# Kernel tuning notes

Measured on AMD Instinct MI355X. Metric: run time of the kernel, lower is better.

## Reference

```python
import jax, jax.numpy as jnp
import numpy as np

DIM = 1024
E = 8
K = 2
EPS = 1e-5

def _ln(x, g, b):
    mu = jnp.mean(x, axis=-1, keepdims=True)
    var = jnp.mean(jnp.square(x - mu), axis=-1, keepdims=True)
    return (x - mu) * jax.lax.rsqrt(var + EPS) * g + b

def setup_inputs() -> dict:
    key = jax.random.key(0)
    ks = jax.random.split(key, 8)
    H = 2 * DIM
    s_in = 1.0 / np.sqrt(DIM)
    s_h = 1.0 / np.sqrt(H)
    return {
        "x": jax.random.normal(ks[0], (2, 2048, DIM), dtype=jnp.float32),
        "gate_w": jax.random.uniform(ks[1], (DIM, E), minval=-s_in, maxval=s_in, dtype=jnp.float32),
        "w1": jax.random.uniform(ks[2], (E, DIM, H), minval=-s_in, maxval=s_in, dtype=jnp.float32),
        "b1": jax.random.uniform(ks[3], (E, H), minval=-s_in, maxval=s_in, dtype=jnp.float32),
        "ln1_g": jnp.ones((E, H), dtype=jnp.float32),
        "ln1_b": jnp.zeros((E, H), dtype=jnp.float32),
        "w2": jax.random.uniform(ks[4], (E, H, DIM), minval=-s_h, maxval=s_h, dtype=jnp.float32),
        "b2": jax.random.uniform(ks[5], (E, DIM), minval=-s_h, maxval=s_h, dtype=jnp.float32),
        "ln_g": jnp.ones((DIM,), dtype=jnp.float32),
        "ln_b": jnp.zeros((DIM,), dtype=jnp.float32),
    }

def reference(x, gate_w, w1, b1, ln1_g, ln1_b, w2, b2, ln_g, ln_b):
    shape = x.shape
    xf = x.reshape(-1, shape[-1])                      # [T, D]
    gates = jax.nn.softmax(xf @ gate_w, axis=-1)       # [T, E]
    topw, topi = jax.lax.top_k(gates, K)               # [T, K]
    topw = topw / jnp.sum(topw, axis=-1, keepdims=True)
    # combine weights per expert: [T, E]
    combine = jnp.sum(topw[:, :, None] * jax.nn.one_hot(topi, E, dtype=xf.dtype), axis=1)
    # run all experts on all tokens (vectorized grouped GEMM), combine by gate mask
    h = jnp.einsum('td,edh->teh', xf, w1) + b1          # [T, E, 2D]
    h = _ln(h, ln1_g, ln1_b)
    h = jax.nn.gelu(h, approximate=False)
    y = jnp.einsum('teh,ehd->ted', h, w2) + b2          # [T, E, D]
    out = jnp.einsum('ted,te->td', y, combine)          # [T, D]
    out = _ln(out + xf, ln_g, ln_b)
    return out.reshape(shape)
```

## Files before the change

### kernel.cpp

```cpp
#include <hip/hip_runtime.h>
#include <hip/hip_bf16.h>

#define DIMX 1024
#define HID  2048
#define NE   8
#define NT   4096
#define NPAIR 8192
#define MAXSTRIP 72

typedef __attribute__((ext_vector_type(8))) __bf16 bf16x8;
typedef __attribute__((ext_vector_type(4))) float f32x4;

__device__ inline unsigned short f2bf(float f) {
  union { float f; unsigned u; } v; v.f = f;
  unsigned r = v.u + 0x7FFFu + ((v.u >> 16) & 1u);
  return (unsigned short)(r >> 16);
}
__device__ inline float bf2f(unsigned short h) {
  union { unsigned u; float f; } v; v.u = ((unsigned)h) << 16;
  return v.f;
}

__device__ __forceinline__ void gload_lds16(const unsigned short* g, unsigned short* l) {
  __builtin_amdgcn_global_load_lds(
      (const __attribute__((address_space(1))) unsigned int*)g,
      (__attribute__((address_space(3))) unsigned int*)l, 16, 0, 0);
}

#define O_CNT   0u
#define O_TOK   1024u
#define O_TK    132096u
#define O_PW    263168u
#define O_TI    394240u
#define O_TW    427008u
#define O_POFF  459776u
#define O_SE    459904u
#define O_SR0   460416u
#define O_XBF   524288u
#define O_W1T   16777216u
#define O_W2T   50331648u
#define O_H     83886080u
#define O_Y     121634816u

__global__ __launch_bounds__(256) void k_gate_cvt(const float* __restrict__ x,
                                                  const float* __restrict__ gw,
                                                  unsigned short* __restrict__ xbf,
                                                  int* __restrict__ ti,
                                                  float* __restrict__ tw) {
  int t = blockIdx.x * 4 + (threadIdx.x >> 6);
  int lane = threadIdx.x & 63;
  const float4* xr = (const float4*)(x + (size_t)t * DIMX);
  ushort4* xo = (ushort4*)(xbf + (size_t)t * DIMX);
  float p[NE];
#pragma unroll
  for (int e = 0; e < NE; e++) p[e] = 0.f;
#pragma unroll
  for (int j = 0; j < 4; j++) {
    int idx4 = j * 64 + lane;
    float4 v = xr[idx4];
    ushort4 o; o.x = f2bf(v.x); o.y = f2bf(v.y); o.z = f2bf(v.z); o.w = f2bf(v.w);
    xo[idx4] = o;
    const float4* gp = (const float4*)(gw + (size_t)(idx4 * 4) * NE);
    float4 gA = gp[0], gB = gp[1], gC = gp[2], gD = gp[3];
    float4 gE = gp[4], gF = gp[5], gG = gp[6], gH = gp[7];
    p[0] += v.x * gA.x + v.y * gC.x + v.z * gE.x + v.w * gG.x;
    p[1] += v.x * gA.y + v.y * gC.y + v.z * gE.y + v.w * gG.y;
    p[2] += v.x * gA.z + v.y * gC.z + v.z * gE.z + v.w * gG.z;
    p[3] += v.x * gA.w + v.y * gC.w + v.z * gE.w + v.w * gG.w;
    p[4] += v.x * gB.x + v.y * gD.x + v.z * gF.x + v.w * gH.x;
    p[5] += v.x * gB.y + v.y * gD.y + v.z * gF.y + v.w * gH.y;
    p[6] += v.x * gB.z + v.y * gD.z + v.z * gF.z + v.w * gH.z;
    p[7] += v.x * gB.w + v.y * gD.w + v.z * gF.w + v.w * gH.w;
  }
#pragma unroll
  for (int e = 0; e < NE; e++)
#pragma unroll
    for (int off = 32; off > 0; off >>= 1) p[e] += __shfl_xor(p[e], off);
  if (lane == 0) {
    int ia = 0; float va = p[0];
#pragma unroll
    for (int e = 1; e < NE; e++) if (p[e] > va) { va = p[e]; ia = e; }
    int ib = -1; float vb = -3.0e38f;
#pragma unroll
    for (int e = 0; e < NE; e++) { if (e == ia) continue; if (p[e] > vb) { vb = p[e]; ib = e; } }
    float w0 = 1.f / (1.f + expf(vb - va));
    ti[t * 2] = ia;     tw[t * 2] = w0;
    ti[t * 2 + 1] = ib; tw[t * 2 + 1] = 1.f - w0;
  }
}

__global__ __launch_bounds__(512) void k_build(const int* __restrict__ ti,
                                               const float* __restrict__ tw,
                                               int* __restrict__ cnt,
                                               int* __restrict__ poffs,
                                               int* __restrict__ s_e, int* __restrict__ s_r0,
                                               int* __restrict__ ptok, int* __restrict__ ptk,
                                               float* __restrict__ pw) {
  __shared__ int sti[NPAIR];
  __shared__ float stw[NPAIR];
  __shared__ int scnt[NE];
  for (int i = threadIdx.x; i < NPAIR; i += 512) { sti[i] = ti[i]; stw[i] = tw[i]; }
  __syncthreads();
  int wid = threadIdx.x >> 6;
  int lane = threadIdx.x & 63;
  int c = 0;
  for (int p = lane; p < NPAIR; p += 64) c += (sti[p] == wid) ? 1 : 0;
#pragma unroll
  for (int off = 32; off > 0; off >>= 1) c += __shfl_xor(c, off);
  if (lane == 0) scnt[wid] = c;
  __syncthreads();
  if (threadIdx.x == 0) {
    int s = 0, pacc = 0;
    for (int e = 0; e < NE; e++) {
      cnt[e] = scnt[e];
      poffs[e] = pacc;
      int ns = (scnt[e] + 127) >> 7;
      for (int k = 0; k < ns; k++) { s_e[s] = e; s_r0[s] = k * 128; s++; }
      pacc += ns * 128;
    }
    poffs[NE] = pacc;
    for (; s < MAXSTRIP; s++) { s_e[s] = -1; s_r0[s] = 0; }
  }
  int base = 0;
  for (int p0 = 0; p0 < NPAIR; p0 += 64) {
    int p = p0 + lane;
    bool m = (sti[p] == wid);
    unsigned long long mask = __ballot(m);
    if (m) {
      int pos = base + __popcll(mask & ((1ull << lane) - 1ull));
      ptok[wid * NT + pos] = p >> 1;
      ptk[wid * NT + pos] = p;
      pw[wid * NT + pos] = stw[p];
    }
    base += __popcll(mask);
  }
}

__global__ __launch_bounds__(256) void k_transpose_cvt(const float* __restrict__ in,
                                                       unsigned short* __restrict__ out,
                                                       int R, int C) {
  __shared__ float tile[64][73];
  int e = blockIdx.z;
  const float* ip = in + (size_t)e * R * C;
  unsigned short* op = out + (size_t)e * R * C;
  int c0 = blockIdx.x * 64, r0 = blockIdx.y * 64;
  int tx = threadIdx.x & 15, ty = threadIdx.x >> 4;
#pragma unroll
  for (int i = 0; i < 4; i++) {
    int row = ty + i * 16;
    float4 v = *(const float4*)(ip + (size_t)(r0 + row) * C + c0 + tx * 4);
    tile[row][tx * 4] = v.x; tile[row][tx * 4 + 1] = v.y;
    tile[row][tx * 4 + 2] = v.z; tile[row][tx * 4 + 3] = v.w;
  }
  __syncthreads();
  int rx = threadIdx.x & 15, cy = threadIdx.x >> 4;
  int r_off = rx * 4;
#pragma unroll
  for (int i = 0; i < 4; i++) {
    int cc = cy + i * 16;
    ushort4 h;
    h.x = f2bf(tile[r_off][cc]);     h.y = f2bf(tile[r_off + 1][cc]);
    h.z = f2bf(tile[r_off + 2][cc]); h.w = f2bf(tile[r_off + 3][cc]);
    *(ushort4*)(op + (size_t)(c0 + cc) * R + r0 + r_off) = h;
  }
}

#define BM 128
#define BN 128
#define BK 32
#define KSTEPS 32

__global__ __launch_bounds__(256) void k_gemm1(
    const unsigned short* __restrict__ xbf,
    const unsigned short* __restrict__ w1t,
    const float* __restrict__ bias1,
    const int* __restrict__ cnt, const int* __restrict__ s_e,
    const int* __restrict__ s_r0, const int* __restrict__ poffs,
    const int* __restrict__ ptok,
    unsigned short* __restrict__ hpre)
{
  int lid = blockIdx.x + 16 * blockIdx.y;
  int xcd = lid & 7;
  int t4 = lid >> 3;
  int colb = t4 & 15;
  int s = xcd * 9 + (t4 >> 4);
  int e = s_e[s];
  if (e < 0) return;
  int r0e = s_r0[s];
  int n_e = cnt[e];
  int pbase = poffs[e];
  int col0 = colb * BN;

  __shared__ __align__(16) unsigned short As[3][BM][BK];
  __shared__ __align__(16) unsigned short Bs[3][BN][BK];

  int tid = threadIdx.x;
  int lane = tid & 63, wid = tid >> 6;
  int wr = wid >> 1, wc = wid & 1;
  int quad = lane >> 4, m16 = lane & 15;

  int rr = lane >> 2;
  int csrc = ((lane & 3) ^ ((lane >> 3) & 3)) * 8;
  int ga0 = r0e + wid * 32 + rr;      if (ga0 >= n_e) ga0 = n_e - 1;
  int ga1 = r0e + wid * 32 + 16 + rr; if (ga1 >= n_e) ga1 = n_e - 1;
  int t0 = ptok[e * NT + ga0];
  int t1 = ptok[e * NT + ga1];
  const unsigned short* a0p = xbf + (size_t)t0 * DIMX + csrc;
  const unsigned short* a1p = xbf + (size_t)t1 * DIMX + csrc;
  const unsigned short* bbase = w1t + (size_t)e * HID * DIMX;
  const unsigned short* b0p = bbase + (size_t)(col0 + wid * 32 + rr) * DIMX + csrc;
  const unsigned short* b1p = bbase + (size_t)(col0 + wid * 32 + 16 + rr) * DIMX + csrc;

  int ca = (quad ^ ((m16 >> 1) & 3)) * 8;

  f32x4 acc[4][4];
#pragma unroll
  for (int i = 0; i < 4; i++)
#pragma unroll
    for (int j = 0; j < 4; j++) acc[i][j] = (f32x4)(0.f);

#define STAGE1(b, kk) do { \
    gload_lds16(a0p + (kk), &As[b][wid * 32][0]); \
    gload_lds16(a1p + (kk), &As[b][wid * 32 + 16][0]); \
    gload_lds16(b0p + (kk), &Bs[b][wid * 32][0]); \
    gload_lds16(b1p + (kk), &Bs[b][wid * 32 + 16][0]); \
  } while (0)

  STAGE1(0, 0);
  int cur = 0;
  for (int k = 0; k < KSTEPS; ++k) {
    int nxt = (cur == 2) ? 0 : cur + 1;
    if (k + 1 < KSTEPS) {
      STAGE1(nxt, (k + 1) * BK);
      asm volatile("s_waitcnt vmcnt(4)" ::: "memory");
    } else {
      asm volatile("s_waitcnt vmcnt(0)" ::: "memory");
    }
    asm volatile("s_waitcnt lgkmcnt(0)" ::: "memory");
    __builtin_amdgcn_sched_barrier(0);
    __builtin_amdgcn_s_barrier();
    __builtin_amdgcn_sched_barrier(0);
    bf16x8 af[4], bfr[4];
#pragma unroll
    for (int i = 0; i < 4; i++) af[i]  = *(const bf16x8*)&As[cur][wr * 64 + i * 16 + m16][ca];
#pragma unroll
    for (int j = 0; j < 4; j++) bfr[j] = *(const bf16x8*)&Bs[cur][wc * 64 + j * 16 + m16][ca];
    __builtin_amdgcn_s_setprio(1);
#pragma unroll
    for (int i = 0; i < 4; i++)
#pragma unroll
      for (int j = 0; j < 4; j++)
        acc[i][j] = __builtin_amdgcn_mfma_f32_16x16x32_bf16(af[i], bfr[j], acc[i][j], 0, 0, 0);
    __builtin_amdgcn_s_setprio(0);
    cur = nxt;
  }
#undef STAGE1

  float bj[4];
#pragma unroll
  for (int j = 0; j < 4; j++) bj[j] = bias1[e * HID + col0 + wc * 64 + j * 16 + m16];
#pragma unroll
  for (int i = 0; i < 4; i++) {
#pragma unroll
    for (int r = 0; r < 4; r++) {
      int g = r0e + wr * 64 + i * 16 + quad * 4 + r;
      if (g < n_e) {
        size_t rowbase = (size_t)(pbase + g) * HID;
#pragma unroll
        for (int j = 0; j < 4; j++) {
          int colg = col0 + wc * 64 + j * 16 + m16;
          hpre[rowbase + colg] = f2bf(acc[i][j][r] + bj[j]);
        }
      }
    }
  }
}

__global__ __launch_bounds__(256) void k_ln_gelu(unsigned short* __restrict__ h,
                                                 const float* __restrict__ g1,
                                                 const float* __restrict__ bb1,
                                                 const int* __restrict__ s_e) {
  int row = blockIdx.x * 4 + (threadIdx.x >> 6);
  int e = s_e[row >> 7];
  if (e < 0) return;
  int lane = threadIdx.x & 63;
  unsigned short* p = h + (size_t)row * HID;
  int4* p4 = (int4*)p;
  int4 raw[4];
#pragma unroll
  for (int sg = 0; sg < 4; sg++) raw[sg] = p4[sg * 64 + lane];
  float v[32];
#pragma unroll
  for (int sg = 0; sg < 4; sg++) {
    const unsigned short* u = (const unsigned short*)&raw[sg];
#pragma unroll
    for (int k = 0; k < 8; k++) v[sg * 8 + k] = bf2f(u[k]);
  }
  float s = 0.f;
#pragma unroll
  for (int i = 0; i < 32; i++) s += v[i];
#pragma unroll
  for (int off = 32; off > 0; off >>= 1) s += __shfl_xor(s, off);
  float mean = s * (1.f / HID);
  float sq = 0.f;
#pragma unroll
  for (int i = 0; i < 32; i++) { float d = v[i] - mean; sq += d * d; }
#pragma unroll
  for (int off = 32; off > 0; off >>= 1) sq += __shfl_xor(sq, off);
  float rstd = rsqrtf(sq * (1.f / HID) + 1e-5f);
  const float4* gg = (const float4*)(g1 + (size_t)e * HID);
  const float4* gb = (const float4*)(bb1 + (size_t)e * HID);
#pragma unroll
  for (int sg = 0; sg < 4; sg++) {
    float4 ga = gg[sg * 128 + lane * 2], gc = gg[sg * 128 + lane * 2 + 1];
    float4 ba = gb[sg * 128 + lane * 2], bc = gb[sg * 128 + lane * 2 + 1];
    float gn[8] = {ga.x, ga.y, ga.z, ga.w, gc.x, gc.y, gc.z, gc.w};
    float bn[8] = {ba.x, ba.y, ba.z, ba.w, bc.x, bc.y, bc.z, bc.w};
    unsigned short o[8];
#pragma unroll
    for (int k = 0; k < 8; k++) {
      float xn = (v[sg * 8 + k] - mean) * rstd * gn[k] + bn[k];
      float ge = 0.5f * xn * (1.f + erff(xn * 0.7071067811865476f));
      o[k] = f2bf(ge);
    }
    p4[sg * 64 + lane] = *(const int4*)o;
  }
}

__global__ __launch_bounds__(256) void k_gemm2(
    const unsigned short* __restrict__ hb,
    const unsigned short* __restrict__ w2t,
    const float* __restrict__ bias2,
    const int* __restrict__ cnt, const int* __restrict__ s_e,
    const int* __restrict__ s_r0, const int* __restrict__ poffs,
    const int* __restrict__ ptk, const float* __restrict__ pw,
    float* __restrict__ ybufA, float* __restrict__ ybufB)
{
  int lid = blockIdx.x + 8 * (blockIdx.y + 72 * blockIdx.z);
  int xcd = lid & 7;
  int t4 = lid >> 3;
  int colb = t4 & 7;
  int rem = t4 >> 3;
  int ks = rem & 1;
  int s = xcd * 9 + (rem >> 1);
  int e = s_e[s];
  if (e < 0) return;
  int r0e = s_r0[s];
  int n_e = cnt[e];
  int pbase = poffs[e];
  int col0 = colb * BN;
  int kbase = ks << 10;

  __shared__ __align__(16) unsigned short As[3][BM][BK];
  __shared__ __align__(16) unsigned short Bs[3][BN][BK];

  int tid = threadIdx.x;
  int lane = tid & 63, wid = tid >> 6;
  int wr = wid >> 1, wc = wid & 1;
  int quad = lane >> 4, m16 = lane & 15;

  int rr = lane >> 2;
  int csrc = ((lane & 3) ^ ((lane >> 3) & 3)) * 8;
  int ga0 = r0e + wid * 32 + rr;      if (ga0 >= n_e) ga0 = n_e - 1;
  int ga1 = r0e + wid * 32 + 16 + rr; if (ga1 >= n_e) ga1 = n_e - 1;
  const unsigned short* a0p = hb + (size_t)(pbase + ga0) * HID + kbase + csrc;
  const unsigned short* a1p = hb + (size_t)(pbase + ga1) * HID + kbase + csrc;
  const unsigned short* bbase = w2t + (size_t)e * DIMX * HID;
  const unsigned short* b0p = bbase + (size_t)(col0 + wid * 32 + rr) * HID + kbase + csrc;
  const unsigned short* b1p = bbase + (size_t)(col0 + wid * 32 + 16 + rr) * HID + kbase + csrc;

  int ca = (quad ^ ((m16 >> 1) & 3)) * 8;

  f32x4 acc[4][4];
#pragma unroll
  for (int i = 0; i < 4; i++)
#pragma unroll
    for (int j = 0; j < 4; j++) acc[i][j] = (f32x4)(0.f);

#define STAGE2(b, kk) do { \
    gload_lds16(a0p + (kk), &As[b][wid * 32][0]); \
    gload_lds16(a1p + (kk), &As[b][wid * 32 + 16][0]); \
    gload_lds16(b0p + (kk), &Bs[b][wid * 32][0]); \
    gload_lds16(b1p + (kk), &Bs[b][wid * 32 + 16][0]); \
  } while (0)

  STAGE2(0, 0);
  int cur = 0;
  for (int k = 0; k < KSTEPS; ++k) {
    int nxt = (cur == 2) ? 0 : cur + 1;
    if (k + 1 < KSTEPS) {
      STAGE2(nxt, (k + 1) * BK);
      asm volatile("s_waitcnt vmcnt(4)" ::: "memory");
    } else {
      asm volatile("s_waitcnt vmcnt(0)" ::: "memory");
    }
    asm volatile("s_waitcnt lgkmcnt(0)" ::: "memory");
    __builtin_amdgcn_sched_barrier(0);
    __builtin_amdgcn_s_barrier();
    __builtin_amdgcn_sched_barrier(0);
    bf16x8 af[4], bfr[4];
#pragma unroll
    for (int i = 0; i < 4; i++) af[i]  = *(const bf16x8*)&As[cur][wr * 64 + i * 16 + m16][ca];
#pragma unroll
    for (int j = 0; j < 4; j++) bfr[j] = *(const bf16x8*)&Bs[cur][wc * 64 + j * 16 + m16][ca];
    __builtin_amdgcn_s_setprio(1);
#pragma unroll
    for (int i = 0; i < 4; i++)
#pragma unroll
      for (int j = 0; j < 4; j++)
        acc[i][j] = __builtin_amdgcn_mfma_f32_16x16x32_bf16(af[i], bfr[j], acc[i][j], 0, 0, 0);
    __builtin_amdgcn_s_setprio(0);
    cur = nxt;
  }
#undef STAGE2

  float* yb = ks ? ybufB : ybufA;
  float bj[4];
#pragma unroll
  for (int j = 0; j < 4; j++)
    bj[j] = ks ? bias2[e * DIMX + col0 + wc * 64 + j * 16 + m16] : 0.f;
#pragma unroll
  for (int i = 0; i < 4; i++) {
#pragma unroll
    for (int r = 0; r < 4; r++) {
      int g = r0e + wr * 64 + i * 16 + quad * 4 + r;
      if (g < n_e) {
        int pi = e * NT + g;
        float w = pw[pi];
        size_t obase = (size_t)ptk[pi] * DIMX;
#pragma unroll
        for (int j = 0; j < 4; j++) {
          int colg = col0 + wc * 64 + j * 16 + m16;
          yb[obase + colg] = (acc[i][j][r] + bj[j]) * w;
        }
      }
    }
  }
}

__global__ __launch_bounds__(256) void k_final(const float* __restrict__ ybA,
                                               const float* __restrict__ ybB,
                                               const float* __restrict__ x,
                                               const float* __restrict__ lg,
                                               const float* __restrict__ lb,
                                               float* __restrict__ out) {
  int t = blockIdx.x * 4 + (threadIdx.x >> 6);
  int lane = threadIdx.x & 63;
  const float4* yA0 = (const float4*)(ybA + (size_t)t * 2 * DIMX);
  const float4* yA1 = yA0 + DIMX / 4;
  const float4* yB0 = (const float4*)(ybB + (size_t)t * 2 * DIMX);
  const float4* yB1 = yB0 + DIMX / 4;
  const float4* x4 = (const float4*)(x + (size_t)t * DIMX);
  float4 v[4];
  float s = 0.f;
#pragma unroll
  for (int sg = 0; sg < 4; sg++) {
    int idx = sg * 64 + lane;
    float4 a = yA0[idx], b = yA1[idx], a2 = yB0[idx], b2 = yB1[idx], c = x4[idx];
    v[sg].x = a.x + b.x + a2.x + b2.x + c.x;
    v[sg].y = a.y + b.y + a2.y + b2.y + c.y;
    v[sg].z = a.z + b.z + a2.z + b2.z + c.z;
    v[sg].w = a.w + b.w + a2.w + b2.w + c.w;
    s += v[sg].x + v[sg].y + v[sg].z + v[sg].w;
  }
#pragma unroll
  for (int off = 32; off > 0; off >>= 1) s += __shfl_xor(s, off);
  float mean = s * (1.f / DIMX);
  float sq = 0.f;
#pragma unroll
  for (int sg = 0; sg < 4; sg++) {
    float dx = v[sg].x - mean, dy = v[sg].y - mean, dz = v[sg].z - mean, dw = v[sg].w - mean;
    sq += dx * dx + dy * dy + dz * dz + dw * dw;
  }
#pragma unroll
  for (int off = 32; off > 0; off >>= 1) sq += __shfl_xor(sq, off);
  float rstd = rsqrtf(sq * (1.f / DIMX) + 1e-5f);
  float4* o4 = (float4*)(out + (size_t)t * DIMX);
#pragma unroll
  for (int sg = 0; sg < 4; sg++) {
    int idx = sg * 64 + lane;
    float4 g = ((const float4*)lg)[idx], bb = ((const float4*)lb)[idx];
    float4 o;
    o.x = (v[sg].x - mean) * rstd * g.x + bb.x;
    o.y = (v[sg].y - mean) * rstd * g.y + bb.y;
    o.z = (v[sg].z - mean) * rstd * g.z + bb.z;
    o.w = (v[sg].w - mean) * rstd * g.w + bb.w;
    o4[idx] = o;
  }
}

extern "C" void kernel_launch(void* const* d_in, const int* in_sizes, int n_in,
                              void* d_out, int out_size, void* d_ws, size_t ws_size,
                              hipStream_t stream) {
  const float* x     = (const float*)d_in[0];
  const float* gw    = (const float*)d_in[1];
  const float* w1    = (const float*)d_in[2];
  const float* b1    = (const float*)d_in[3];
  const float* ln1g  = (const float*)d_in[4];
  const float* ln1b  = (const float*)d_in[5];
  const float* w2    = (const float*)d_in[6];
  const float* b2    = (const float*)d_in[7];
  const float* lng   = (const float*)d_in[8];
  const float* lnb   = (const float*)d_in[9];
  float* out = (float*)d_out;

  char* ws = (char*)d_ws;
  int* cnt   = (int*)(ws + O_CNT);
  int* ptok  = (int*)(ws + O_TOK);
  int* ptk   = (int*)(ws + O_TK);
  float* pw  = (float*)(ws + O_PW);
  int* ti    = (int*)(ws + O_TI);
  float* tw  = (float*)(ws + O_TW);
  int* poffs = (int*)(ws + O_POFF);
  int* s_e   = (int*)(ws + O_SE);
  int* s_r0  = (int*)(ws + O_SR0);
  unsigned short* xbf  = (unsigned short*)(ws + O_XBF);
  unsigned short* w1t  = (unsigned short*)(ws + O_W1T);
  unsigned short* w2t  = (unsigned short*)(ws + O_W2T);
  unsigned short* hpre = (unsigned short*)(ws + O_H);
  float* ybufA = (float*)(ws + O_Y);
  float* ybufB = (float*)(ws + O_W1T);

  hipLaunchKernelGGL(k_gate_cvt, dim3(NT / 4), dim3(256), 0, stream, x, gw, xbf, ti, tw);
  hipLaunchKernelGGL(k_build, dim3(1), dim3(512), 0, stream, ti, tw, cnt, poffs, s_e, s_r0,
                     ptok, ptk, pw);
  hipLaunchKernelGGL(k_transpose_cvt, dim3(HID / 64, DIMX / 64, NE), dim3(256), 0, stream,
                     w1, w1t, DIMX, HID);
  hipLaunchKernelGGL(k_transpose_cvt, dim3(DIMX / 64, HID / 64, NE), dim3(256), 0, stream,
                     w2, w2t, HID, DIMX);
  hipLaunchKernelGGL(k_gemm1, dim3(HID / BN, MAXSTRIP), dim3(256), 0, stream,
                     xbf, w1t, b1, cnt, s_e, s_r0, poffs, ptok, hpre);
  hipLaunchKernelGGL(k_ln_gelu, dim3(MAXSTRIP * BM / 4), dim3(256), 0, stream,
                     hpre, ln1g, ln1b, s_e);
  hipLaunchKernelGGL(k_gemm2, dim3(DIMX / BN, MAXSTRIP, 2), dim3(256), 0, stream,
                     hpre, w2t, b2, cnt, s_e, s_r0, poffs, ptk, pw, ybufA, ybufB);
  hipLaunchKernelGGL(k_final, dim3(NT / 4), dim3(256), 0, stream, ybufA, ybufB, x, lng, lnb, out);
}
```

Measured before the change: 375.3 us.

## Double K tile to 64 with double-buffered LDS pipeline in both GEMMs

Both grouped GEMM kernels now use a K tile of 64 with two LDS buffers instead of 32 with three. The global-to-LDS load pattern and the XOR swizzle are reworked for 8-row groups, and each iteration issues two MFMA half-steps. This halves the number of barrier/waitcnt iterations and raises MFMA work per sync. In exchange there is less prefetch depth, an extra barrier before each stage, and the LDS footprint grows from 48KB to 64KB, which may reduce occupancy.

```diff
diff --git a/kernel.cpp b/kernel.cpp
--- a/kernel.cpp
+++ b/kernel.cpp
@@ -167,8 +167,8 @@
 
 #define BM 128
 #define BN 128
-#define BK 32
-#define KSTEPS 32
+#define BK 64
+#define KSTEPS 16
 
 __global__ __launch_bounds__(256) void k_gemm1(
     const unsigned short* __restrict__ xbf,
@@ -191,27 +191,29 @@
   int pbase = poffs[e];
   int col0 = colb * BN;
 
-  __shared__ __align__(16) unsigned short As[3][BM][BK];
-  __shared__ __align__(16) unsigned short Bs[3][BN][BK];
+  __shared__ __align__(16) unsigned short As[2][BM][BK];
+  __shared__ __align__(16) unsigned short Bs[2][BN][BK];
 
   int tid = threadIdx.x;
   int lane = tid & 63, wid = tid >> 6;
   int wr = wid >> 1, wc = wid & 1;
   int quad = lane >> 4, m16 = lane & 15;
 
-  int rr = lane >> 2;
-  int csrc = ((lane & 3) ^ ((lane >> 3) & 3)) * 8;
-  int ga0 = r0e + wid * 32 + rr;      if (ga0 >= n_e) ga0 = n_e - 1;
-  int ga1 = r0e + wid * 32 + 16 + rr; if (ga1 >= n_e) ga1 = n_e - 1;
-  int t0 = ptok[e * NT + ga0];
-  int t1 = ptok[e * NT + ga1];
-  const unsigned short* a0p = xbf + (size_t)t0 * DIMX + csrc;
-  const unsigned short* a1p = xbf + (size_t)t1 * DIMX + csrc;
-  const unsigned short* bbase = w1t + (size_t)e * HID * DIMX;
-  const unsigned short* b0p = bbase + (size_t)(col0 + wid * 32 + rr) * DIMX + csrc;
-  const unsigned short* b1p = bbase + (size_t)(col0 + wid * 32 + 16 + rr) * DIMX + csrc;
-
-  int ca = (quad ^ ((m16 >> 1) & 3)) * 8;
+  int r8 = lane >> 3;
+  int csrc = ((lane & 7) ^ r8) * 8;
+  const unsigned short* ap[4];
+  const unsigned short* bp[4];
+  {
+    const unsigned short* bbase = w1t + (size_t)e * HID * DIMX;
+#pragma unroll
+    for (int i = 0; i < 4; i++) {
+      int ga = r0e + wid * 32 + i * 8 + r8; if (ga >= n_e) ga = n_e - 1;
+      ap[i] = xbf + (size_t)ptok[e * NT + ga] * DIMX + csrc;
+      bp[i] = bbase + (size_t)(col0 + wid * 32 + i * 8 + r8) * DIMX + csrc;
+    }
+  }
+
+  int ca0 = (quad ^ (m16 & 7)) * 8;
 
   f32x4 acc[4][4];
 #pragma unroll
@@ -220,31 +222,36 @@
     for (int j = 0; j < 4; j++) acc[i][j] = (f32x4)(0.f);
 
 #define STAGE1(b, kk) do { \
-    gload_lds16(a0p + (kk), &As[b][wid * 32][0]); \
-    gload_lds16(a1p + (kk), &As[b][wid * 32 + 16][0]); \
-    gload_lds16(b0p + (kk), &Bs[b][wid * 32][0]); \
-    gload_lds16(b1p + (kk), &Bs[b][wid * 32 + 16][0]); \
+    gload_lds16(ap[0] + (kk), &As[b][wid * 32 +  0][0]); \
+    gload_lds16(ap[1] + (kk), &As[b][wid * 32 +  8][0]); \
+    gload_lds16(ap[2] + (kk), &As[b][wid * 32 + 16][0]); \
+    gload_lds16(ap[3] + (kk), &As[b][wid * 32 + 24][0]); \
+    gload_lds16(bp[0] + (kk), &Bs[b][wid * 32 +  0][0]); \
+    gload_lds16(bp[1] + (kk), &Bs[b][wid * 32 +  8][0]); \
+    gload_lds16(bp[2] + (kk), &Bs[b][wid * 32 + 16][0]); \
+    gload_lds16(bp[3] + (kk), &Bs[b][wid * 32 + 24][0]); \
   } while (0)
 
   STAGE1(0, 0);
   int cur = 0;
   for (int k = 0; k < KSTEPS; ++k) {
-    int nxt = (cur == 2) ? 0 : cur + 1;
+    asm volatile("s_waitcnt lgkmcnt(0)" ::: "memory");
+    __builtin_amdgcn_sched_barrier(0);
+    __builtin_amdgcn_s_barrier();
     if (k + 1 < KSTEPS) {
-      STAGE1(nxt, (k + 1) * BK);
-      asm volatile("s_waitcnt vmcnt(4)" ::: "memory");
+      STAGE1(cur ^ 1, (k + 1) * BK);
+      asm volatile("s_waitcnt vmcnt(8)" ::: "memory");
     } else {
       asm volatile("s_waitcnt vmcnt(0)" ::: "memory");
     }
-    asm volatile("s_waitcnt lgkmcnt(0)" ::: "memory");
     __builtin_amdgcn_sched_barrier(0);
     __builtin_amdgcn_s_barrier();
     __builtin_amdgcn_sched_barrier(0);
     bf16x8 af[4], bfr[4];
 #pragma unroll
-    for (int i = 0; i < 4; i++) af[i]  = *(const bf16x8*)&As[cur][wr * 64 + i * 16 + m16][ca];
-#pragma unroll
-    for (int j = 0; j < 4; j++) bfr[j] = *(const bf16x8*)&Bs[cur][wc * 64 + j * 16 + m16][ca];
+    for (int i = 0; i < 4; i++) af[i]  = *(const bf16x8*)&As[cur][wr * 64 + i * 16 + m16][ca0];
+#pragma unroll
+    for (int j = 0; j < 4; j++) bfr[j] = *(const bf16x8*)&Bs[cur][wc * 64 + j * 16 + m16][ca0];
     __builtin_amdgcn_s_setprio(1);
 #pragma unroll
     for (int i = 0; i < 4; i++)
@@ -252,7 +259,19 @@
       for (int j = 0; j < 4; j++)
         acc[i][j] = __builtin_amdgcn_mfma_f32_16x16x32_bf16(af[i], bfr[j], acc[i][j], 0, 0, 0);
     __builtin_amdgcn_s_setprio(0);
-    cur = nxt;
+    bf16x8 ag[4], bgr[4];
+#pragma unroll
+    for (int i = 0; i < 4; i++) ag[i]  = *(const bf16x8*)&As[cur][wr * 64 + i * 16 + m16][ca0 ^ 32];
+#pragma unroll
+    for (int j = 0; j < 4; j++) bgr[j] = *(const bf16x8*)&Bs[cur][wc * 64 + j * 16 + m16][ca0 ^ 32];
+    __builtin_amdgcn_s_setprio(1);
+#pragma unroll
+    for (int i = 0; i < 4; i++)
+#pragma unroll
+      for (int j = 0; j < 4; j++)
+        acc[i][j] = __builtin_amdgcn_mfma_f32_16x16x32_bf16(ag[i], bgr[j], acc[i][j], 0, 0, 0);
+    __builtin_amdgcn_s_setprio(0);
+    cur ^= 1;
   }
 #undef STAGE1
 
@@ -351,25 +370,29 @@
   int col0 = colb * BN;
   int kbase = ks << 10;
 
-  __shared__ __align__(16) unsigned short As[3][BM][BK];
-  __shared__ __align__(16) unsigned short Bs[3][BN][BK];
+  __shared__ __align__(16) unsigned short As[2][BM][BK];
+  __shared__ __align__(16) unsigned short Bs[2][BN][BK];
 
   int tid = threadIdx.x;
   int lane = tid & 63, wid = tid >> 6;
   int wr = wid >> 1, wc = wid & 1;
   int quad = lane >> 4, m16 = lane & 15;
 
-  int rr = lane >> 2;
-  int csrc = ((lane & 3) ^ ((lane >> 3) & 3)) * 8;
-  int ga0 = r0e + wid * 32 + rr;      if (ga0 >= n_e) ga0 = n_e - 1;
-  int ga1 = r0e + wid * 32 + 16 + rr; if (ga1 >= n_e) ga1 = n_e - 1;
-  const unsigned short* a0p = hb + (size_t)(pbase + ga0) * HID + kbase + csrc;
-  const unsigned short* a1p = hb + (size_t)(pbase + ga1) * HID + kbase + csrc;
-  const unsigned short* bbase = w2t + (size_t)e * DIMX * HID;
-  const unsigned short* b0p = bbase + (size_t)(col0 + wid * 32 + rr) * HID + kbase + csrc;
-  const unsigned short* b1p = bbase + (size_t)(col0 + wid * 32 + 16 + rr) * HID + kbase + csrc;
-
-  int ca = (quad ^ ((m16 >> 1) & 3)) * 8;
+  int r8 = lane >> 3;
+  int csrc = ((lane & 7) ^ r8) * 8;
+  const unsigned short* ap[4];
+  const unsigned short* bp[4];
+  {
+    const unsigned short* bbase = w2t + (size_t)e * DIMX * HID;
+#pragma unroll
+    for (int i = 0; i < 4; i++) {
+      int ga = r0e + wid * 32 + i * 8 + r8; if (ga >= n_e) ga = n_e - 1;
+      ap[i] = hb + (size_t)(pbase + ga) * HID + kbase + csrc;
+      bp[i] = bbase + (size_t)(col0 + wid * 32 + i * 8 + r8) * HID + kbase + csrc;
+    }
+  }
+
+  int ca0 = (quad ^ (m16 & 7)) * 8;
 
   f32x4 acc[4][4];
 #pragma unroll
@@ -378,31 +401,36 @@
     for (int j = 0; j < 4; j++) acc[i][j] = (f32x4)(0.f);
 
 #define STAGE2(b, kk) do { \
-    gload_lds16(a0p + (kk), &As[b][wid * 32][0]); \
-    gload_lds16(a1p + (kk), &As[b][wid * 32 + 16][0]); \
-    gload_lds16(b0p + (kk), &Bs[b][wid * 32][0]); \
-    gload_lds16(b1p + (kk), &Bs[b][wid * 32 + 16][0]); \
+    gload_lds16(ap[0] + (kk), &As[b][wid * 32 +  0][0]); \
+    gload_lds16(ap[1] + (kk), &As[b][wid * 32 +  8][0]); \
+    gload_lds16(ap[2] + (kk), &As[b][wid * 32 + 16][0]); \
+    gload_lds16(ap[3] + (kk), &As[b][wid * 32 + 24][0]); \
+    gload_lds16(bp[0] + (kk), &Bs[b][wid * 32 +  0][0]); \
+    gload_lds16(bp[1] + (kk), &Bs[b][wid * 32 +  8][0]); \
+    gload_lds16(bp[2] + (kk), &Bs[b][wid * 32 + 16][0]); \
+    gload_lds16(bp[3] + (kk), &Bs[b][wid * 32 + 24][0]); \
   } while (0)
 
   STAGE2(0, 0);
   int cur = 0;
   for (int k = 0; k < KSTEPS; ++k) {
-    int nxt = (cur == 2) ? 0 : cur + 1;
+    asm volatile("s_waitcnt lgkmcnt(0)" ::: "memory");
+    __builtin_amdgcn_sched_barrier(0);
+    __builtin_amdgcn_s_barrier();
     if (k + 1 < KSTEPS) {
-      STAGE2(nxt, (k + 1) * BK);
-      asm volatile("s_waitcnt vmcnt(4)" ::: "memory");
+      STAGE2(cur ^ 1, (k + 1) * BK);
+      asm volatile("s_waitcnt vmcnt(8)" ::: "memory");
     } else {
       asm volatile("s_waitcnt vmcnt(0)" ::: "memory");
     }
-    asm volatile("s_waitcnt lgkmcnt(0)" ::: "memory");
     __builtin_amdgcn_sched_barrier(0);
     __builtin_amdgcn_s_barrier();
     __builtin_amdgcn_sched_barrier(0);
     bf16x8 af[4], bfr[4];
 #pragma unroll
-    for (int i = 0; i < 4; i++) af[i]  = *(const bf16x8*)&As[cur][wr * 64 + i * 16 + m16][ca];
-#pragma unroll
-    for (int j = 0; j < 4; j++) bfr[j] = *(const bf16x8*)&Bs[cur][wc * 64 + j * 16 + m16][ca];
+    for (int i = 0; i < 4; i++) af[i]  = *(const bf16x8*)&As[cur][wr * 64 + i * 16 + m16][ca0];
+#pragma unroll
+    for (int j = 0; j < 4; j++) bfr[j] = *(const bf16x8*)&Bs[cur][wc * 64 + j * 16 + m16][ca0];
     __builtin_amdgcn_s_setprio(1);
 #pragma unroll
     for (int i = 0; i < 4; i++)
@@ -410,7 +438,19 @@
       for (int j = 0; j < 4; j++)
         acc[i][j] = __builtin_amdgcn_mfma_f32_16x16x32_bf16(af[i], bfr[j], acc[i][j], 0, 0, 0);
     __builtin_amdgcn_s_setprio(0);
-    cur = nxt;
+    bf16x8 ag[4], bgr[4];
+#pragma unroll
+    for (int i = 0; i < 4; i++) ag[i]  = *(const bf16x8*)&As[cur][wr * 64 + i * 16 + m16][ca0 ^ 32];
+#pragma unroll
+    for (int j = 0; j < 4; j++) bgr[j] = *(const bf16x8*)&Bs[cur][wc * 64 + j * 16 + m16][ca0 ^ 32];
+    __builtin_amdgcn_s_setprio(1);
+#pragma unroll
+    for (int i = 0; i < 4; i++)
+#pragma unroll
+      for (int j = 0; j < 4; j++)
+        acc[i][j] = __builtin_amdgcn_mfma_f32_16x16x32_bf16(ag[i], bgr[j], acc[i][j], 0, 0, 0);
+    __builtin_amdgcn_s_setprio(0);
+    cur ^= 1;
   }
 #undef STAGE2
 
```

Measured after the change: 383.0 us. 1.02x slower.
